# Performance work log

Hardware: AMD Instinct MI355X
Metric: run time of the kernel (lower is better)

Reference implementation:

```python
import jax, jax.numpy as jnp
import numpy as np

B, H0, W0, DIM, HEADS, WS, SHIFT = 32, 56, 56, 384, 12, 7, 3
MLP_HID = DIM * 4
N = WS * WS  # tokens per window

def _rel_pos_index(ws):
    coords = np.stack(np.meshgrid(np.arange(ws), np.arange(ws), indexing='ij')).reshape(2, -1)
    rel = (coords[:, :, None] - coords[:, None, :]).transpose(1, 2, 0)
    rel[:, :, 0] += ws - 1
    rel[:, :, 1] += ws - 1
    rel[:, :, 0] *= 2 * ws - 1
    return rel.sum(-1)  # (N, N) int

REL_IDX = _rel_pos_index(WS)

def _shift_mask(H, W, ws, shift):
    # standard Swin SW-MSA mask: 0 within same region, -100 across regions
    img = np.zeros((H, W), dtype=np.int32)
    cnt = 0
    for hs in (slice(0, -ws), slice(-ws, -shift), slice(-shift, None)):
        for wsl in (slice(0, -ws), slice(-ws, -shift), slice(-shift, None)):
            img[hs, wsl] = cnt
            cnt += 1
    mw = img.reshape(H // ws, ws, W // ws, ws).transpose(0, 2, 1, 3).reshape(-1, ws * ws)
    return np.where(mw[:, None, :] != mw[:, :, None], -100.0, 0.0).astype(np.float32)  # (nW, N, N)

MASK = _shift_mask(H0, W0, WS, SHIFT)

def _ln(x, g, b, eps=1e-5):
    m = x.mean(-1, keepdims=True)
    v = ((x - m) ** 2).mean(-1, keepdims=True)
    return (x - m) / jnp.sqrt(v + eps) * g + b

def setup_inputs():
    key = jax.random.key(0)
    ks = jax.random.split(key, 8)
    d = {}
    d['x'] = jax.random.normal(ks[0], (B, H0 * W0, DIM), jnp.float32)
    d['H'], d['W'] = H0, W0
    d['norm1_g'] = jnp.ones((DIM,), jnp.float32)
    d['norm1_b'] = jnp.zeros((DIM,), jnp.float32)
    d['qkv_w'] = jax.random.normal(ks[1], (3 * DIM, DIM), jnp.float32) * 0.02
    d['qkv_b'] = jnp.zeros((3 * DIM,), jnp.float32)
    d['rpb_table'] = jax.random.normal(ks[2], ((2 * WS - 1) ** 2, HEADS), jnp.float32) * 0.02
    d['proj_w'] = jax.random.normal(ks[3], (DIM, DIM), jnp.float32) * 0.02
    d['proj_b'] = jnp.zeros((DIM,), jnp.float32)
    d['norm2_g'] = jnp.ones((DIM,), jnp.float32)
    d['norm2_b'] = jnp.zeros((DIM,), jnp.float32)
    d['fc1_w'] = jax.random.normal(ks[4], (MLP_HID, DIM), jnp.float32) * 0.02
    d['fc1_b'] = jnp.zeros((MLP_HID,), jnp.float32)
    d['fc2_w'] = jax.random.normal(ks[5], (DIM, MLP_HID), jnp.float32) * 0.02
    d['fc2_b'] = jnp.zeros((DIM,), jnp.float32)
    return d

def reference(x, H, W, norm1_g, norm1_b, qkv_w, qkv_b, rpb_table, proj_w, proj_b, norm2_g, norm2_b, fc1_w, fc1_b, fc2_w, fc2_b):
    Bx, L, C = x.shape
    hd = C // HEADS
    scale = hd ** -0.5
    shortcut = x
    xn = _ln(x, norm1_g, norm1_b).reshape(Bx, H, W, C)
    if SHIFT > 0:
        xn = jnp.roll(xn, (-SHIFT, -SHIFT), axis=(1, 2))
    nWh, nWw = H // WS, W // WS
    nW = nWh * nWw
    # window partition: (B, H, W, C) -> (B*nW, N, C)
    xw = xn.reshape(Bx, nWh, WS, nWw, WS, C).transpose(0, 1, 3, 2, 4, 5).reshape(-1, N, C)
    qkv = (xw @ qkv_w.T + qkv_b).reshape(-1, N, 3, HEADS, hd).transpose(2, 0, 3, 1, 4)
    q, k, v = qkv[0] * scale, qkv[1], qkv[2]  # (B*nW, HEADS, N, hd)
    attn = jnp.einsum('bhnd,bhmd->bhnm', q, k)
    bias = rpb_table[jnp.asarray(REL_IDX.reshape(-1))].reshape(N, N, HEADS).transpose(2, 0, 1)
    attn = attn + bias[None]
    if SHIFT > 0:
        attn = attn.reshape(Bx, nW, HEADS, N, N) + jnp.asarray(MASK)[None, :, None]
        attn = attn.reshape(-1, HEADS, N, N)
    attn = jax.nn.softmax(attn, axis=-1)
    out = jnp.einsum('bhnm,bhmd->bhnd', attn, v).transpose(0, 2, 1, 3).reshape(-1, N, C)
    out = out @ proj_w.T + proj_b
    # window reverse: (B*nW, N, C) -> (B, H, W, C)
    xr = out.reshape(Bx, nWh, nWw, WS, WS, C).transpose(0, 1, 3, 2, 4, 5).reshape(Bx, H, W, C)
    if SHIFT > 0:
        xr = jnp.roll(xr, (SHIFT, SHIFT), axis=(1, 2))
    x = shortcut + xr.reshape(Bx, L, C)
    h = _ln(x, norm2_g, norm2_b)
    h = jax.nn.gelu(h @ fc1_w.T + fc1_b, approximate=False)  # nn.GELU default = exact erf
    h = h @ fc2_w.T + fc2_b
    return x + h
```

## Files before the change

### kernel.cpp

```cpp
#include <hip/hip_runtime.h>
#include <hip/hip_bf16.h>

#define C_DIM   384
#define HEADS   12
#define HDIM    32
#define NTOK    49
#define TOT_WIN 2048
#define M_TOK   100352
#define QKV_N   1152
#define MLP_N   1536
#define SHIFT_V 3

typedef __bf16 bf16x8_t __attribute__((ext_vector_type(8)));
typedef float  f32x4_t  __attribute__((ext_vector_type(4)));

__device__ inline float b2f(ushort u) {
    union { unsigned u; float f; } p; p.u = ((unsigned)u) << 16; return p.f;
}
__device__ inline ushort f2b(float f) {
    union { float f; unsigned u; } p; p.f = f;
    unsigned r = p.u + 0x7FFF + ((p.u >> 16) & 1);
    return (ushort)(r >> 16);
}
__device__ inline float ldin(const void* p, size_t i, int dt) {
    return dt ? b2f(((const ushort*)p)[i]) : ((const float*)p)[i];
}

__device__ inline void gload_lds16(const ushort* g, ushort* l) {
    __builtin_amdgcn_global_load_lds(
        (__attribute__((address_space(1))) void*)const_cast<ushort*>(g),
        (__attribute__((address_space(3))) void*)l, 16, 0, 0);
}

__device__ inline int win2tok(int grow) {
    int widx = grow / 49, tok = grow - widx * 49;
    int b = widx >> 6, w_ = widx & 63;
    int wh = w_ >> 3, ww = w_ & 7;
    int r = tok / 7, c = tok - r * 7;
    int h = wh * 7 + r + SHIFT_V; if (h >= 56) h -= 56;
    int wc = ww * 7 + c + SHIFT_V; if (wc >= 56) wc -= 56;
    return b * 3136 + h * 56 + wc;
}

__global__ void sniff_kernel(const ushort* x16, int* flag) {
    const int tid = threadIdx.x;
    int cnt = 0;
    for (int i = tid; i < 4096; i += 256) {
        ushort u = x16[2 * i];
        int e = (u >> 7) & 0xFF;
        if ((u & 0x7FFF) == 0 || (e >= 107 && e <= 147)) cnt++;
    }
    __shared__ int ss[256];
    ss[tid] = cnt; __syncthreads();
    for (int s = 128; s; s >>= 1) { if (tid < s) ss[tid] += ss[tid + s]; __syncthreads(); }
    if (tid == 0) *flag = (ss[0] >= 2048) ? 1 : 0;
}

__global__ void cvt_w_kernel(const void* src, ushort* dst, int n, const int* flagp) {
    const int dt = *flagp;
    for (int i = blockIdx.x * blockDim.x + threadIdx.x; i < n; i += gridDim.x * blockDim.x)
        dst[i] = dt ? ((const ushort*)src)[i] : f2b(((const float*)src)[i]);
}

__global__ void cvt_p_kernel(const void* n1g, const void* n1b, const void* qkvb,
                             const void* projb, const void* n2g, const void* n2b,
                             const void* fc1b, const void* fc2b, const void* rpb,
                             float* prm, const int* flagp) {
    const int dt = *flagp;
    for (int i = threadIdx.x; i < 7020; i += 256) {
        float v;
        if      (i < 384)  v = ldin(n1g,  i,        dt);
        else if (i < 768)  v = ldin(n1b,  i - 384,  dt);
        else if (i < 1920) v = ldin(qkvb, i - 768,  dt);
        else if (i < 2304) v = ldin(projb,i - 1920, dt);
        else if (i < 2688) v = ldin(n2g,  i - 2304, dt);
        else if (i < 3072) v = ldin(n2b,  i - 2688, dt);
        else if (i < 4608) v = ldin(fc1b, i - 3072, dt);
        else if (i < 4992) v = ldin(fc2b, i - 4608, dt);
        else               v = ldin(rpb,  i - 4992, dt);
        prm[i] = v;
    }
}

template<int MODE>
__global__ __launch_bounds__(256) void ln_kernel(
    const void* __restrict__ x, const float* __restrict__ g,
    const float* __restrict__ b, ushort* __restrict__ out,
    const int* flagp, int moff)
{
    const int dt = *flagp;
    const int wid = threadIdx.x >> 6, lane = threadIdx.x & 63;
    const int m = blockIdx.x * 4 + wid;
    const int src = (MODE == 0) ? win2tok(moff + m) : (moff + m);

    float v[6]; float s = 0.f, sq = 0.f;
    #pragma unroll
    for (int k = 0; k < 6; ++k) {
        size_t idx = (size_t)src * C_DIM + lane + 64 * k;
        v[k] = (MODE == 2) ? b2f(((const ushort*)x)[idx]) : ldin(x, idx, dt);
        s += v[k]; sq += v[k] * v[k];
    }
    #pragma unroll
    for (int off = 32; off; off >>= 1) {
        s  += __shfl_xor(s,  off, 64);
        sq += __shfl_xor(sq, off, 64);
    }
    float mean = s * (1.f / 384.f);
    float var  = sq * (1.f / 384.f) - mean * mean;
    float rstd = rsqrtf(var + 1e-5f);
    #pragma unroll
    for (int k = 0; k < 6; ++k) {
        int col = lane + 64 * k;
        out[(size_t)m * C_DIM + col] =
            f2b((v[k] - mean) * rstd * g[col] + b[col]);
    }
}

template<int MODE>
__global__ __launch_bounds__(256, 2) void gemm_bt(
    const ushort* __restrict__ A, const ushort* __restrict__ W,
    const float* __restrict__ bias, ushort* outb, void* outv,
    const void* resid, const int* flagp, int N, int K, int Mrows, int moff)
{
    __shared__ __align__(16) ushort As[3][128 * 32];
    __shared__ __align__(16) ushort Bs[3][128 * 32];

    const int dt   = *flagp;
    const int tid  = threadIdx.x;
    const int wid  = tid >> 6;
    const int lane = tid & 63;
    const int bm = blockIdx.y * 128;
    const int bn = blockIdx.x * 128;
    const int wm = (wid >> 1) * 64;
    const int wn = (wid & 1) * 64;
    const int lrow = lane & 15;
    const int lk   = (lane >> 4) << 3;

    const int c0    = wid * 2;
    const int srow0 = c0 * 16 + (lane >> 2);
    const int srow1 = srow0 + 16;
    const int skoff = (lane & 3) << 3;

    const int ar0 = (bm + srow0 < Mrows) ? (bm + srow0) : (Mrows - 1);
    const int ar1 = (bm + srow1 < Mrows) ? (bm + srow1) : (Mrows - 1);

    const ushort* pa0 = A + (size_t)ar0 * K + skoff;
    const ushort* pa1 = A + (size_t)ar1 * K + skoff;
    const ushort* pb0 = W + (size_t)(bn + srow0) * K + skoff;
    const ushort* pb1 = W + (size_t)(bn + srow1) * K + skoff;

    float biasf[4]; int coln[4];
    #pragma unroll
    for (int n = 0; n < 4; ++n) {
        coln[n] = bn + wn + n * 16 + lrow;
        biasf[n] = bias[coln[n]];
    }

    f32x4_t acc[4][4];
    #pragma unroll
    for (int m = 0; m < 4; ++m)
        #pragma unroll
        for (int n = 0; n < 4; ++n) acc[m][n] = (f32x4_t){0.f, 0.f, 0.f, 0.f};

    const int nk = K >> 5;
    gload_lds16(pa0,      As[0] + (c0)     * 512);
    gload_lds16(pa1,      As[0] + (c0 + 1) * 512);
    gload_lds16(pb0,      Bs[0] + (c0)     * 512);
    gload_lds16(pb1,      Bs[0] + (c0 + 1) * 512);
    gload_lds16(pa0 + 32, As[1] + (c0)     * 512);
    gload_lds16(pa1 + 32, As[1] + (c0 + 1) * 512);
    gload_lds16(pb0 + 32, Bs[1] + (c0)     * 512);
    gload_lds16(pb1 + 32, Bs[1] + (c0 + 1) * 512);

    int cur = 0, stg = 2;
    for (int kt = 0; kt < nk; ++kt) {
        if (kt + 2 < nk) {
            const int k2 = (kt + 2) << 5;
            gload_lds16(pa0 + k2, As[stg] + (c0)     * 512);
            gload_lds16(pa1 + k2, As[stg] + (c0 + 1) * 512);
            gload_lds16(pb0 + k2, Bs[stg] + (c0)     * 512);
            gload_lds16(pb1 + k2, Bs[stg] + (c0 + 1) * 512);
            __builtin_amdgcn_sched_barrier(0);
            asm volatile("s_waitcnt vmcnt(8)" ::: "memory");
        } else if (kt + 1 < nk) {
            __builtin_amdgcn_sched_barrier(0);
            asm volatile("s_waitcnt vmcnt(4)" ::: "memory");
        } else {
            asm volatile("s_waitcnt vmcnt(0)" ::: "memory");
        }
        __builtin_amdgcn_s_barrier();
        __builtin_amdgcn_sched_barrier(0);

        bf16x8_t af[4], bfr[4];
        #pragma unroll
        for (int m = 0; m < 4; ++m)
            af[m] = *(const bf16x8_t*)&As[cur][(wm + m * 16 + lrow) * 32 + lk];
        #pragma unroll
        for (int n = 0; n < 4; ++n)
            bfr[n] = *(const bf16x8_t*)&Bs[cur][(wn + n * 16 + lrow) * 32 + lk];
        #pragma unroll
        for (int m = 0; m < 4; ++m)
            #pragma unroll
            for (int n = 0; n < 4; ++n)
                acc[m][n] = __builtin_amdgcn_mfma_f32_16x16x32_bf16(
                    af[m], bfr[n], acc[m][n], 0, 0, 0);

        __builtin_amdgcn_sched_barrier(0);
        __builtin_amdgcn_s_barrier();
        cur = (cur == 2) ? 0 : cur + 1;
        stg = (stg == 2) ? 0 : stg + 1;
    }

    const int rbase = bm + wm + ((lane >> 4) << 2);
    #pragma unroll
    for (int m = 0; m < 4; ++m) {
        #pragma unroll
        for (int j = 0; j < 4; ++j) {
            int grow = rbase + m * 16 + j;
            if (grow >= Mrows) continue;
            #pragma unroll
            for (int n = 0; n < 4; ++n) {
                float v = acc[m][n][j] + biasf[n];
                if (MODE == 0) {
                    outb[(size_t)grow * N + coln[n]] = f2b(v);
                } else if (MODE == 2) {
                    v = 0.5f * v * (1.0f + erff(v * 0.70710678118654752f));
                    outb[(size_t)grow * N + coln[n]] = f2b(v);
                } else if (MODE == 1) {
                    size_t oidx = (size_t)win2tok(moff + grow) * (size_t)N + coln[n];
                    outb[oidx] = f2b(v + ldin(resid, oidx, dt));
                } else {
                    size_t oidx = (size_t)(moff + grow) * (size_t)N + coln[n];
                    float r = v + b2f(((const ushort*)resid)[oidx]);
                    if (dt) ((ushort*)outv)[oidx] = f2b(r);
                    else    ((float*) outv)[oidx] = r;
                }
            }
        }
    }
}

__global__ __launch_bounds__(256) void attn_kernel(
    const ushort* __restrict__ qkv, const float* __restrict__ rpb,
    ushort* __restrict__ out, int win_off)
{
    __shared__ __align__(16) ushort Pl[4][64 * 64];
    __shared__ __align__(16) ushort Vtl[4][32 * 64];

    const int tid = threadIdx.x, wid = tid >> 6, lane = tid & 63;
    const int lo = lane & 15, hi = lane >> 4;
    const int widx = blockIdx.x;
    const int w_ = (win_off + widx) & 63;
    const int wh = w_ >> 3, ww = w_ & 7;
    const bool edge = (wh == 7) || (ww == 7);

    char* P  = (char*)Pl[wid];
    char* Vw = (char*)Vtl[wid];

    int qr[4], qc[4], rq[4];
    #pragma unroll
    for (int n = 0; n < 4; ++n) {
        int q = n * 16 + lo; if (q > 48) q = 48;
        qr[n] = q / 7; qc[n] = q - qr[n] * 7;
        int gh = wh * 7 + qr[n], gw = ww * 7 + qc[n];
        rq[n] = (gh < 49 ? 0 : (gh < 53 ? 1 : 2)) * 3 + (gw < 49 ? 0 : (gw < 53 ? 1 : 2));
    }

    for (int h = wid; h < HEADS; h += 4) {
        const size_t hb = (size_t)widx * 49 * QKV_N + h * HDIM;

        bf16x8_t kf[4], qf[4];
        #pragma unroll
        for (int t = 0; t < 4; ++t) {
            int r = t * 16 + lo;
            bf16x8_t z = {};
            kf[t] = z; qf[t] = z;
            if (r < 49) {
                kf[t] = *(const bf16x8_t*)(qkv + hb + (size_t)r * QKV_N + 384 + hi * 8);
                qf[t] = *(const bf16x8_t*)(qkv + hb + (size_t)r * QKV_N + hi * 8);
            }
        }

        {
            const int kk = lane;
            union { bf16x8_t v; ushort u[8]; } vv[4];
            #pragma unroll
            for (int c = 0; c < 4; ++c) {
                bf16x8_t z = {};
                vv[c].v = (kk < 49) ? *(const bf16x8_t*)(qkv + hb + (size_t)kk * QKV_N + 768 + c * 8)
                                    : z;
            }
            #pragma unroll
            for (int d = 0; d < 32; ++d) {
                int byo = (d * 128 + kk * 2) ^ ((d & 7) << 4);
                *(ushort*)(Vw + byo) = vv[d >> 3].u[d & 7];
            }
        }

        f32x4_t St[4][4];
        #pragma unroll
        for (int m = 0; m < 4; ++m)
            #pragma unroll
            for (int n = 0; n < 4; ++n) St[m][n] = (f32x4_t){0.f, 0.f, 0.f, 0.f};
        #pragma unroll
        for (int m = 0; m < 4; ++m)
            #pragma unroll
            for (int n = 0; n < 4; ++n)
                St[m][n] = __builtin_amdgcn_mfma_f32_16x16x32_bf16(kf[m], qf[n], St[m][n], 0, 0, 0);

        #pragma unroll
        for (int m = 0; m < 4; ++m) {
            #pragma unroll
            for (int j = 0; j < 4; ++j) {
                const int kk = m * 16 + hi * 4 + j;
                const int kcl = (kk > 48) ? 48 : kk;
                const int kr = kcl / 7, kc = kcl - kr * 7;
                int rk = 0;
                if (edge) {
                    int gh = wh * 7 + kr, gw = ww * 7 + kc;
                    rk = (gh < 49 ? 0 : (gh < 53 ? 1 : 2)) * 3 + (gw < 49 ? 0 : (gw < 53 ? 1 : 2));
                }
                #pragma unroll
                for (int n = 0; n < 4; ++n) {
                    int idx = (qr[n] - kr + 6) * 13 + (qc[n] - kc + 6);
                    float v = St[m][n][j] * 0.17677669529663687f + rpb[idx * 12 + h];
                    if (edge && (rq[n] != rk)) v -= 100.f;
                    if (kk > 48) v = -1e30f;
                    St[m][n][j] = v;
                }
            }
        }

        float sm[4];
        #pragma unroll
        for (int n = 0; n < 4; ++n) {
            float mv = St[0][n][0];
            #pragma unroll
            for (int m = 0; m < 4; ++m)
                #pragma unroll
                for (int j = 0; j < 4; ++j) mv = fmaxf(mv, St[m][n][j]);
            mv = fmaxf(mv, __shfl_xor(mv, 16, 64));
            mv = fmaxf(mv, __shfl_xor(mv, 32, 64));
            float sv = 0.f;
            #pragma unroll
            for (int m = 0; m < 4; ++m)
                #pragma unroll
                for (int j = 0; j < 4; ++j) {
                    float e = __expf(St[m][n][j] - mv);
                    St[m][n][j] = e; sv += e;
                }
            sv += __shfl_xor(sv, 16, 64);
            sv += __shfl_xor(sv, 32, 64);
            sm[n] = 1.f / sv;
        }

        #pragma unroll
        for (int m = 0; m < 4; ++m) {
            #pragma unroll
            for (int n = 0; n < 4; ++n) {
                union { ushort4 u4; __bf16 b[4]; } pk;
                #pragma unroll
                for (int j = 0; j < 4; ++j) pk.b[j] = (__bf16)(St[m][n][j] * sm[n]);
                int byo = ((n * 16 + lo) * 128 + (m * 16 + hi * 4) * 2) ^ ((lo & 7) << 4);
                *(ushort4*)(P + byo) = pk.u4;
            }
        }

        f32x4_t Oa[4][2];
        #pragma unroll
        for (int mt = 0; mt < 4; ++mt)
            #pragma unroll
            for (int nt = 0; nt < 2; ++nt) Oa[mt][nt] = (f32x4_t){0.f, 0.f, 0.f, 0.f};
        #pragma unroll
        for (int s = 0; s < 2; ++s) {
            bf16x8_t vf[2];
            #pragma unroll
            for (int nt = 0; nt < 2; ++nt) {
                int byo = ((nt * 16 + lo) * 128 + s * 64 + hi * 16) ^ ((lo & 7) << 4);
                vf[nt] = *(const bf16x8_t*)(Vw + byo);
            }
            #pragma unroll
            for (int mt = 0; mt < 4; ++mt) {
                int byo = ((mt * 16 + lo) * 128 + s * 64 + hi * 16) ^ ((lo & 7) << 4);
                bf16x8_t pf = *(const bf16x8_t*)(P + byo);
                #pragma unroll
                for (int nt = 0; nt < 2; ++nt)
                    Oa[mt][nt] = __builtin_amdgcn_mfma_f32_16x16x32_bf16(pf, vf[nt], Oa[mt][nt], 0, 0, 0);
            }
        }

        #pragma unroll
        for (int mt = 0; mt < 4; ++mt) {
            #pragma unroll
            for (int j = 0; j < 4; ++j) {
                int q = mt * 16 + hi * 4 + j;
                if (q < 49) {
                    size_t ro = ((size_t)(widx * 49 + q)) * C_DIM + h * HDIM;
                    #pragma unroll
                    for (int nt = 0; nt < 2; ++nt)
                        out[ro + nt * 16 + lo] = f2b(Oa[mt][nt][j]);
                }
            }
        }
    }
}

extern "C" void kernel_launch(void* const* d_in, const int* in_sizes, int n_in,
                              void* d_out, int out_size, void* d_ws, size_t ws_size,
                              hipStream_t stream)
{
    const void* x      = d_in[0];
    const void* n1g    = d_in[3];
    const void* n1b    = d_in[4];
    const void* qkv_w  = d_in[5];
    const void* qkv_b  = d_in[6];
    const void* rpb    = d_in[7];
    const void* proj_w = d_in[8];
    const void* proj_b = d_in[9];
    const void* n2g    = d_in[10];
    const void* n2b    = d_in[11];
    const void* fc1_w  = d_in[12];
    const void* fc1_b  = d_in[13];
    const void* fc2_w  = d_in[14];
    const void* fc2_b  = d_in[15];

    int*    flagp = (int*)d_ws;
    float*  prm   = (float*)((char*)d_ws + 256);
    ushort* wq    = (ushort*)((char*)d_ws + 28416);
    ushort* wp    = wq + 442368;
    ushort* w1m   = wp + 147456;
    ushort* w2m   = w1m + 589824;
    const size_t WSTATIC = 3567360;
    const size_t X2B_B   = 77070336ull;

    int nc = 64;
    const int opts[7] = {1, 2, 4, 8, 16, 32, 64};
    for (int i = 0; i < 7; ++i) {
        size_t need = WSTATIC + X2B_B + ((size_t)M_TOK / opts[i]) * 3840ull;
        if (need <= ws_size) { nc = opts[i]; break; }
    }
    const int wins_pc = TOT_WIN / nc;
    const int rows_pc = wins_pc * NTOK;
    const int gx      = (rows_pc + 127) / 128;

    ushort* x2b = (ushort*)((char*)d_ws + WSTATIC);
    ushort* ws0 = x2b + (size_t)M_TOK * C_DIM;
    ushort* ws1 = ws0 + (size_t)rows_pc * C_DIM;

    sniff_kernel<<<1, 256, 0, stream>>>((const ushort*)x, flagp);
    cvt_p_kernel<<<1, 256, 0, stream>>>(n1g, n1b, qkv_b, proj_b, n2g, n2b,
                                        fc1_b, fc2_b, rpb, prm, flagp);
    cvt_w_kernel<<<432, 256, 0, stream>>>(qkv_w,  wq,  442368, flagp);
    cvt_w_kernel<<<144, 256, 0, stream>>>(proj_w, wp,  147456, flagp);
    cvt_w_kernel<<<576, 256, 0, stream>>>(fc1_w,  w1m, 589824, flagp);
    cvt_w_kernel<<<576, 256, 0, stream>>>(fc2_w,  w2m, 589824, flagp);

    const float* b_qkv = prm + 768;
    const float* b_prj = prm + 1920;
    const float* b_fc1 = prm + 3072;
    const float* b_fc2 = prm + 4608;
    const float* rpb_c = prm + 4992;

    for (int c = 0; c < nc; ++c) {
        const int moff = c * rows_pc;
        ln_kernel<0><<<rows_pc / 4, 256, 0, stream>>>(x, prm + 0, prm + 384, ws0, flagp, moff);
        gemm_bt<0><<<dim3(9, gx), 256, 0, stream>>>(
            ws0, wq, b_qkv, ws1, nullptr, nullptr, flagp, QKV_N, C_DIM, rows_pc, 0);
        attn_kernel<<<wins_pc, 256, 0, stream>>>(ws1, rpb_c, ws0, c * wins_pc);
        gemm_bt<1><<<dim3(3, gx), 256, 0, stream>>>(
            ws0, wp, b_prj, x2b, nullptr, x, flagp, C_DIM, C_DIM, rows_pc, moff);
    }

    for (int c = 0; c < nc; ++c) {
        const int moff = c * rows_pc;
        ln_kernel<2><<<rows_pc / 4, 256, 0, stream>>>(x2b, prm + 2304, prm + 2688, ws0, flagp, moff);
        gemm_bt<2><<<dim3(12, gx), 256, 0, stream>>>(
            ws0, w1m, b_fc1, ws1, nullptr, nullptr, flagp, MLP_N, C_DIM, rows_pc, 0);
        gemm_bt<3><<<dim3(3, gx), 256, 0, stream>>>(
            ws1, w2m, b_fc2, nullptr, d_out, x2b, flagp, C_DIM, MLP_N, rows_pc, moff);
    }
}
```

Measured before the change: 1.156 ms.

## Enlarge GEMM tile to 256x128 with 8 waves and double buffering

The GEMM block tile grows from 128x128 with 4 waves to 256x128 with 8 waves (512 threads), so each weight tile loaded into LDS is reused across twice as many rows. The triple-buffered LDS pipeline is cut to a double buffer with a one-stage prefetch, and the load mapping is simplified to one row per thread group. The trade-off is less prefetch depth, fewer blocks in flight per CU, and more rows lost to padding in the last M tile.

```diff
diff --git a/kernel.cpp b/kernel.cpp
--- a/kernel.cpp
+++ b/kernel.cpp
@@ -117,37 +117,34 @@
 }
 
 template<int MODE>
-__global__ __launch_bounds__(256, 2) void gemm_bt(
+__global__ __launch_bounds__(512) void gemm_bt(
     const ushort* __restrict__ A, const ushort* __restrict__ W,
     const float* __restrict__ bias, ushort* outb, void* outv,
     const void* resid, const int* flagp, int N, int K, int Mrows, int moff)
 {
-    __shared__ __align__(16) ushort As[3][128 * 32];
-    __shared__ __align__(16) ushort Bs[3][128 * 32];
+    __shared__ __align__(16) ushort As[2][256 * 32];
+    __shared__ __align__(16) ushort Bs[2][128 * 32];
 
     const int dt   = *flagp;
     const int tid  = threadIdx.x;
     const int wid  = tid >> 6;
     const int lane = tid & 63;
-    const int bm = blockIdx.y * 128;
+    const int bm = blockIdx.y * 256;
     const int bn = blockIdx.x * 128;
     const int wm = (wid >> 1) * 64;
     const int wn = (wid & 1) * 64;
     const int lrow = lane & 15;
     const int lk   = (lane >> 4) << 3;
 
-    const int c0    = wid * 2;
-    const int srow0 = c0 * 16 + (lane >> 2);
-    const int srow1 = srow0 + 16;
-    const int skoff = (lane & 3) << 3;
-
-    const int ar0 = (bm + srow0 < Mrows) ? (bm + srow0) : (Mrows - 1);
-    const int ar1 = (bm + srow1 < Mrows) ? (bm + srow1) : (Mrows - 1);
-
-    const ushort* pa0 = A + (size_t)ar0 * K + skoff;
-    const ushort* pa1 = A + (size_t)ar1 * K + skoff;
-    const ushort* pb0 = W + (size_t)(bn + srow0) * K + skoff;
-    const ushort* pb1 = W + (size_t)(bn + srow1) * K + skoff;
+    const int arow = tid >> 2;
+    const int koff = (tid & 3) << 3;
+    const int ar0 = (bm + arow       < Mrows) ? (bm + arow)       : (Mrows - 1);
+    const int ar1 = (bm + 128 + arow < Mrows) ? (bm + 128 + arow) : (Mrows - 1);
+    const int brow = bn + arow;
+
+    const ushort* pa0 = A + (size_t)ar0 * K + koff;
+    const ushort* pa1 = A + (size_t)ar1 * K + koff;
+    const ushort* pb  = W + (size_t)brow * K + koff;
 
     float biasf[4]; int coln[4];
     #pragma unroll
@@ -163,28 +160,20 @@
         for (int n = 0; n < 4; ++n) acc[m][n] = (f32x4_t){0.f, 0.f, 0.f, 0.f};
 
     const int nk = K >> 5;
-    gload_lds16(pa0,      As[0] + (c0)     * 512);
-    gload_lds16(pa1,      As[0] + (c0 + 1) * 512);
-    gload_lds16(pb0,      Bs[0] + (c0)     * 512);
-    gload_lds16(pb1,      Bs[0] + (c0 + 1) * 512);
-    gload_lds16(pa0 + 32, As[1] + (c0)     * 512);
-    gload_lds16(pa1 + 32, As[1] + (c0 + 1) * 512);
-    gload_lds16(pb0 + 32, Bs[1] + (c0)     * 512);
-    gload_lds16(pb1 + 32, Bs[1] + (c0 + 1) * 512);
-
-    int cur = 0, stg = 2;
+    gload_lds16(pa0, As[0] + tid * 8);
+    gload_lds16(pa1, As[0] + 4096 + tid * 8);
+    gload_lds16(pb,  Bs[0] + tid * 8);
+
+    int cur = 0;
     for (int kt = 0; kt < nk; ++kt) {
-        if (kt + 2 < nk) {
-            const int k2 = (kt + 2) << 5;
-            gload_lds16(pa0 + k2, As[stg] + (c0)     * 512);
-            gload_lds16(pa1 + k2, As[stg] + (c0 + 1) * 512);
-            gload_lds16(pb0 + k2, Bs[stg] + (c0)     * 512);
-            gload_lds16(pb1 + k2, Bs[stg] + (c0 + 1) * 512);
+        if (kt + 1 < nk) {
+            const int nxt = cur ^ 1;
+            const int k1 = (kt + 1) << 5;
+            gload_lds16(pa0 + k1, As[nxt] + tid * 8);
+            gload_lds16(pa1 + k1, As[nxt] + 4096 + tid * 8);
+            gload_lds16(pb  + k1, Bs[nxt] + tid * 8);
             __builtin_amdgcn_sched_barrier(0);
-            asm volatile("s_waitcnt vmcnt(8)" ::: "memory");
-        } else if (kt + 1 < nk) {
-            __builtin_amdgcn_sched_barrier(0);
-            asm volatile("s_waitcnt vmcnt(4)" ::: "memory");
+            asm volatile("s_waitcnt vmcnt(3)" ::: "memory");
         } else {
             asm volatile("s_waitcnt vmcnt(0)" ::: "memory");
         }
@@ -207,8 +196,7 @@
 
         __builtin_amdgcn_sched_barrier(0);
         __builtin_amdgcn_s_barrier();
-        cur = (cur == 2) ? 0 : cur + 1;
-        stg = (stg == 2) ? 0 : stg + 1;
+        cur ^= 1;
     }
 
     const int rbase = bm + wm + ((lane >> 4) << 2);
@@ -441,7 +429,7 @@
     }
     const int wins_pc = TOT_WIN / nc;
     const int rows_pc = wins_pc * NTOK;
-    const int gx      = (rows_pc + 127) / 128;
+    const int gx      = (rows_pc + 255) / 256;
 
     ushort* x2b = (ushort*)((char*)d_ws + WSTATIC);
     ushort* ws0 = x2b + (size_t)M_TOK * C_DIM;
@@ -464,19 +452,19 @@
     for (int c = 0; c < nc; ++c) {
         const int moff = c * rows_pc;
         ln_kernel<0><<<rows_pc / 4, 256, 0, stream>>>(x, prm + 0, prm + 384, ws0, flagp, moff);
-        gemm_bt<0><<<dim3(9, gx), 256, 0, stream>>>(
+        gemm_bt<0><<<dim3(9, gx), 512, 0, stream>>>(
             ws0, wq, b_qkv, ws1, nullptr, nullptr, flagp, QKV_N, C_DIM, rows_pc, 0);
         attn_kernel<<<wins_pc, 256, 0, stream>>>(ws1, rpb_c, ws0, c * wins_pc);
-        gemm_bt<1><<<dim3(3, gx), 256, 0, stream>>>(
+        gemm_bt<1><<<dim3(3, gx), 512, 0, stream>>>(
             ws0, wp, b_prj, x2b, nullptr, x, flagp, C_DIM, C_DIM, rows_pc, moff);
     }
 
     for (int c = 0; c < nc; ++c) {
         const int moff = c * rows_pc;
         ln_kernel<2><<<rows_pc / 4, 256, 0, stream>>>(x2b, prm + 2304, prm + 2688, ws0, flagp, moff);
-        gemm_bt<2><<<dim3(12, gx), 256, 0, stream>>>(
+        gemm_bt<2><<<dim3(12, gx), 512, 0, stream>>>(
             ws0, w1m, b_fc1, ws1, nullptr, nullptr, flagp, MLP_N, C_DIM, rows_pc, 0);
-        gemm_bt<3><<<dim3(3, gx), 256, 0, stream>>>(
+        gemm_bt<3><<<dim3(3, gx), 512, 0, stream>>>(
             ws1, w2m, b_fc2, nullptr, d_out, x2b, flagp, C_DIM, MLP_N, rows_pc, moff);
     }
 }
```

Measured after the change: 1.099 ms (median of 2 runs). 4.9% less time.
